# Kernel optimization log

Measured on AMD Instinct MI355X. Metric: run time of the kernel, lower is better.

## Reference

```python
import jax, jax.numpy as jnp
import numpy as np

IMG, P, C, E = 256, 16, 3, 200
N = (IMG // P) ** 2          # 256 patches
NUM_MASKED = int(N * 0.75)   # 192
PATCH_ELEMS = C * P * P      # 768


def setup_inputs() -> dict:
    key = jax.random.key(0)
    ks = jax.random.split(key, 10)
    B = 128
    x = jax.random.normal(ks[0], (B, C, IMG, IMG), dtype=jnp.float32)
    perm = jax.random.permutation(ks[1], N).astype(jnp.int32)
    conv_w = jax.random.normal(ks[2], (E, C, P, P), dtype=jnp.float32) * 0.02
    conv_b = jnp.zeros((E,), dtype=jnp.float32)
    pos_embed = jax.random.normal(ks[3], (1, N, E), dtype=jnp.float32) * 0.02
    mask_token = jnp.zeros((1, E), dtype=jnp.float32)
    W_enc = jax.random.normal(ks[4], (E, E), dtype=jnp.float32) * (1.0 / np.sqrt(E))
    b_enc = jnp.zeros((E,), dtype=jnp.float32)
    W_dec = jax.random.normal(ks[5], (E, PATCH_ELEMS), dtype=jnp.float32) * (1.0 / np.sqrt(E))
    b_dec = jnp.zeros((PATCH_ELEMS,), dtype=jnp.float32)
    return {"x": x, "conv_w": conv_w, "conv_b": conv_b, "pos_embed": pos_embed,
            "mask_token": mask_token, "W_enc": W_enc, "b_enc": b_enc,
            "W_dec": W_dec, "b_dec": b_dec, "perm": perm}


def _patchify(x):
    # [B,C,H,W] -> [B, N, C*P*P], row-major patch order (matches conv stride=P then flatten)
    B = x.shape[0]
    g = IMG // P
    x = x.reshape(B, C, g, P, g, P)           # B C gh P gw P
    x = x.transpose(0, 2, 4, 1, 3, 5)         # B gh gw C P P
    return x.reshape(B, g * g, C * P * P)


def _fold(patches):
    # [B, N, C*P*P] -> [B,C,H,W]; idx iterates rows (i) outer, cols (j) inner
    B = patches.shape[0]
    g = IMG // P
    p = patches.reshape(B, g, g, C, P, P)
    return p.transpose(0, 3, 1, 4, 2, 5).reshape(B, C, IMG, IMG)


def reference(x, conv_w, conv_b, pos_embed, mask_token, W_enc, b_enc, W_dec, b_dec, perm):
    masked_idx = perm[:NUM_MASKED]
    unmasked_idx = perm[NUM_MASKED:]
    # patch embed (Conv2d k=P, stride=P == linear over flattened patches)
    patches = _patchify(x)                                   # [B,N,768]
    w_flat = conv_w.reshape(E, -1)                           # [E, 768]
    emb = jnp.einsum('bnp,ep->bne', patches, w_flat) + conv_b + pos_embed  # [B,N,E]
    visible = emb[:, unmasked_idx, :]                        # [B, N-192, E]
    encoded = jnp.einsum('bne,ef->bnf', visible, W_enc) + b_enc
    B = x.shape[0]
    full = jnp.zeros((B, N, E), dtype=x.dtype)
    full = full.at[:, unmasked_idx, :].set(encoded)
    full = full.at[:, masked_idx, :].set(jnp.broadcast_to(mask_token, (B, NUM_MASKED, E)))
    full = full + pos_embed
    dec = jnp.einsum('bne,ep->bnp', full, W_dec) + b_dec     # [B,N,768]
    img = _fold(dec)                                         # [B,C,H,W]
    return img, masked_idx
```

## Files before the change

### kernel.cpp

```cpp
#include <hip/hip_runtime.h>

typedef __attribute__((ext_vector_type(8))) __bf16 bf16x8;
typedef __attribute__((ext_vector_type(4))) float f32x4;

constexpr int Bsz   = 128;
constexpr int EE    = 200;
constexpr int EP    = 256;
constexpr int KP    = 224;
constexpr int NMASK = 192;
constexpr int PE    = 768;
constexpr int M1    = Bsz * 64;
constexpr long IMG_ELEMS = (long)Bsz * 3 * 256 * 256;

constexpr int VROWS = 16;
constexpr int VBLK  = M1 / VROWS;
constexpr int FBLK  = NMASK * 4;
constexpr int ASTR  = 776;
constexpr int TSTR  = 264;

__device__ __forceinline__ f32x4 mfma16(bf16x8 a, bf16x8 b, f32x4 c) {
    return __builtin_amdgcn_mfma_f32_16x16x32_bf16(a, b, c, 0, 0, 0);
}

__global__ __launch_bounds__(256) void k_prep(
    const float* __restrict__ pos, const float* __restrict__ wflat,
    const float* __restrict__ Wenc, const float* __restrict__ Wdec,
    const float* __restrict__ conv_b, const float* __restrict__ b_enc,
    const float* __restrict__ b_dec, const float* __restrict__ mask_token,
    const int* __restrict__ perm,
    float* __restrict__ posP, __bf16* __restrict__ W1t,
    __bf16* __restrict__ W2t, __bf16* __restrict__ W3t,
    float* __restrict__ cbp, float* __restrict__ bep,
    float* __restrict__ dec_masked, float* __restrict__ out_idx)
{
    __shared__ float rowv[256];
    int blk = blockIdx.x, t = threadIdx.x;
    if (blk < 256) {
        posP[blk * 256 + t] = (t < EE) ? pos[blk * EE + t] : 0.f;
        return;
    }
    blk -= 256;
    if (blk < 768) {
        int e = blk / 3, k = (blk % 3) * 256 + t;
        W1t[e * 768 + k] = (e < EE) ? (__bf16)wflat[e * 768 + k] : (__bf16)0.f;
        return;
    }
    blk -= 768;
    if (blk < 256) {
        if (t < KP) W2t[blk * KP + t] =
            (blk < EE && t < EE) ? (__bf16)Wenc[t * EE + blk] : (__bf16)0.f;
        return;
    }
    blk -= 256;
    if (blk < 768) {
        if (t < KP) W3t[blk * KP + t] =
            (t < EE) ? (__bf16)Wdec[t * PE + blk] : (__bf16)0.f;
        return;
    }
    blk -= 768;
    if (blk < NMASK) {
        const int i = blk;
        const int n = perm[i];
        rowv[t] = (t < EE) ? (mask_token[t] + pos[n * EE + t]) : 0.f;
        __syncthreads();
        float a0 = b_dec[t], a1 = b_dec[t + 256], a2 = b_dec[t + 512];
        #pragma unroll 4
        for (int k = 0; k < EE; ++k) {
            const float rv = rowv[k];
            a0 = fmaf(rv, Wdec[k * PE + t], a0);
            a1 = fmaf(rv, Wdec[k * PE + t + 256], a1);
            a2 = fmaf(rv, Wdec[k * PE + t + 512], a2);
        }
        dec_masked[i * PE + t]       = a0;
        dec_masked[i * PE + t + 256] = a1;
        dec_masked[i * PE + t + 512] = a2;
        return;
    }
    cbp[t] = (t < EE) ? conv_b[t] : 0.f;
    bep[t] = (t < EE) ? b_enc[t] : 0.f;
    if (t < NMASK) out_idx[t] = (float)perm[t];
}

__global__ __launch_bounds__(512, 4) void k_mega(
    const float* __restrict__ x, const __bf16* __restrict__ W1t,
    const __bf16* __restrict__ W2t, const __bf16* __restrict__ W3t,
    const float* __restrict__ cbp, const float* __restrict__ bep,
    const float* __restrict__ posP, const float* __restrict__ bdec,
    const int* __restrict__ perm, const float* __restrict__ dec_masked,
    float* __restrict__ img)
{
    __shared__ __bf16 smem[VROWS * ASTR];
    __bf16* As    = smem;
    __bf16* vis_t = smem;
    __bf16* ful_t = smem + VROWS * TSTR;
    __shared__ int nidx[VROWS];

    const int t    = threadIdx.x;
    const int grp5 = blockIdx.x / 5, rem5 = blockIdx.x % 5;
    const int lane = t & 63, wid = t >> 6;
    const int quad = lane >> 4, lid = lane & 15;

    if (rem5 >= 2) {
        const int fb  = grp5 * 3 + (rem5 - 2);
        const int i   = fb % NMASK;
        const int grp = fb / NMASK;
        const int n   = perm[i];
        if (t < 384) {
            const int sub = t / 192, f4 = t % 192;
            f32x4 v = *(const f32x4*)&dec_masked[i * PE + f4 * 4];
            const int p = f4 * 4;
            const int c = p >> 8, py = (p >> 4) & 15, px = p & 15;
            const long base = (long)c * 65536 + ((n >> 4) * 16 + py) * 256
                            + (n & 15) * 16 + px;
            const int b0 = grp * 32 + sub * 16;
            #pragma unroll
            for (int bb = 0; bb < 16; ++bb)
                __builtin_nontemporal_store(
                    v, (f32x4*)&img[(long)(b0 + bb) * 3 * 65536 + base]);
        }
        return;
    }

    const int bid  = grp5 * 2 + rem5;
    const int m0   = bid * VROWS;
    const int bimg = m0 >> 6;
    if (t < VROWS) nidx[t] = perm[NMASK + (m0 & 63) + t];

    {
        const int row = t >> 5;
        const int tt  = t & 31;
        const int m = m0 + row;
        const int n = perm[NMASK + (m & 63)];
        const int abase = bimg * 196608 + (n >> 4) * 4096 + (n & 15) * 16;
        #pragma unroll
        for (int it = 0; it < 3; ++it) {
            int k = tt * 8 + it * 256;
            int c = k >> 8, py = (k >> 4) & 15, px = k & 15;
            const float* ap = x + abase + c * 65536 + py * 256 + px;
            f32x4 a0 = __builtin_nontemporal_load((const f32x4*)ap);
            f32x4 a1 = __builtin_nontemporal_load((const f32x4*)(ap + 4));
            bf16x8 av;
            av[0] = (__bf16)a0.x; av[1] = (__bf16)a0.y; av[2] = (__bf16)a0.z; av[3] = (__bf16)a0.w;
            av[4] = (__bf16)a1.x; av[5] = (__bf16)a1.y; av[6] = (__bf16)a1.z; av[7] = (__bf16)a1.w;
            *(bf16x8*)&As[row * ASTR + k] = av;
        }
    }
    __syncthreads();

    const int e0w = wid * 32;
    f32x4 acc1[2] = {};
    const __bf16* b1 = &W1t[e0w * 768 + quad * 8];
    #pragma unroll 8
    for (int k0 = 0; k0 < 768; k0 += 32) {
        bf16x8 a0 = *(const bf16x8*)&As[lid * ASTR + k0 + quad * 8];
        #pragma unroll
        for (int j = 0; j < 2; ++j) {
            bf16x8 bv = *(const bf16x8*)&b1[(j * 16 + lid) * 768 + k0];
            acc1[j] = mfma16(a0, bv, acc1[j]);
        }
    }
    __syncthreads();

    #pragma unroll
    for (int j = 0; j < 2; ++j) {
        const int e = e0w + j * 16 + lid;
        const float cb = cbp[e];
        #pragma unroll
        for (int r = 0; r < 4; ++r) {
            const int ml = quad * 4 + r;
            vis_t[ml * TSTR + e] = (__bf16)(acc1[j][r] + cb + posP[nidx[ml] * 256 + e]);
        }
    }
    __syncthreads();

    f32x4 acc2[2] = {};
    const __bf16* b2 = &W2t[e0w * KP + quad * 8];
    #pragma unroll
    for (int k0 = 0; k0 < KP; k0 += 32) {
        bf16x8 a0 = *(const bf16x8*)&vis_t[lid * TSTR + k0 + quad * 8];
        #pragma unroll
        for (int j = 0; j < 2; ++j) {
            bf16x8 bv = *(const bf16x8*)&b2[(j * 16 + lid) * KP + k0];
            acc2[j] = mfma16(a0, bv, acc2[j]);
        }
    }
    #pragma unroll
    for (int j = 0; j < 2; ++j) {
        const int e = e0w + j * 16 + lid;
        const float be = bep[e];
        #pragma unroll
        for (int r = 0; r < 4; ++r) {
            const int ml = quad * 4 + r;
            ful_t[ml * TSTR + e] = (__bf16)(acc2[j][r] + be + posP[nidx[ml] * 256 + e]);
        }
    }
    __syncthreads();

    f32x4 acc3[6] = {};
    const int p0w = wid * 96;
    const __bf16* b3 = &W3t[p0w * KP + quad * 8];
    #pragma unroll
    for (int k0 = 0; k0 < KP; k0 += 32) {
        bf16x8 a0 = *(const bf16x8*)&ful_t[lid * TSTR + k0 + quad * 8];
        #pragma unroll
        for (int j = 0; j < 6; ++j) {
            bf16x8 bv = *(const bf16x8*)&b3[(j * 16 + lid) * KP + k0];
            acc3[j] = mfma16(a0, bv, acc3[j]);
        }
    }
    #pragma unroll
    for (int j = 0; j < 6; ++j) {
        const int p = p0w + j * 16 + lid;
        const int c = p >> 8, py = (p >> 4) & 15, px = p & 15;
        const float bd = bdec[p];
        const long obase = (long)(bimg * 3 + c) * 65536 + py * 256 + px;
        #pragma unroll
        for (int r = 0; r < 4; ++r) {
            const int n = nidx[quad * 4 + r];
            __builtin_nontemporal_store(
                acc3[j][r] + bd, &img[obase + (n >> 4) * 4096 + (n & 15) * 16]);
        }
    }
}

extern "C" void kernel_launch(void* const* d_in, const int* in_sizes, int n_in,
                              void* d_out, int out_size, void* d_ws, size_t ws_size,
                              hipStream_t stream)
{
    const float* x          = (const float*)d_in[0];
    const float* conv_w     = (const float*)d_in[1];
    const float* conv_b     = (const float*)d_in[2];
    const float* pos        = (const float*)d_in[3];
    const float* mask_token = (const float*)d_in[4];
    const float* W_enc      = (const float*)d_in[5];
    const float* b_enc      = (const float*)d_in[6];
    const float* W_dec      = (const float*)d_in[7];
    const float* b_dec      = (const float*)d_in[8];
    const int*   perm       = (const int*)d_in[9];
    float* out = (float*)d_out;

    __bf16* visible = (__bf16*)d_ws;
    __bf16* full    = visible + M1 * EP;
    __bf16* W1t     = full + (M1 + NMASK) * EP;
    __bf16* W2t     = W1t + 256 * 768;
    __bf16* W3t     = W2t + 256 * KP;
    float*  posP    = (float*)(W3t + 768 * KP);
    float*  cbp     = posP + 256 * 256;
    float*  bep     = cbp + 256;
    float*  decm    = bep + 256;

    k_prep<<<256 + 768 + 256 + 768 + NMASK + 1, 256, 0, stream>>>(
        pos, conv_w, W_enc, W_dec, conv_b, b_enc, b_dec, mask_token, perm,
        posP, W1t, W2t, W3t, cbp, bep, decm, out + IMG_ELEMS);
    k_mega<<<VBLK + FBLK, 512, 0, stream>>>(
        x, W1t, W2t, W3t, cbp, bep, posP, b_dec, perm, decm, out);
}
```

Before: 252.3 us.

## Collapse the three linear layers into one precomputed 768x768 weight plus per-patch bias table

```diff
diff --git a/kernel.cpp b/kernel.cpp
--- a/kernel.cpp
+++ b/kernel.cpp
@@ -5,8 +5,6 @@
 
 constexpr int Bsz   = 128;
 constexpr int EE    = 200;
-constexpr int EP    = 256;
-constexpr int KP    = 224;
 constexpr int NMASK = 192;
 constexpr int PE    = 768;
 constexpr int M1    = Bsz * 64;
@@ -16,58 +14,77 @@
 constexpr int VBLK  = M1 / VROWS;
 constexpr int FBLK  = NMASK * 4;
 constexpr int ASTR  = 776;
-constexpr int TSTR  = 264;
 
 __device__ __forceinline__ f32x4 mfma16(bf16x8 a, bf16x8 b, f32x4 c) {
     return __builtin_amdgcn_mfma_f32_16x16x32_bf16(a, b, c, 0, 0, 0);
 }
 
-__global__ __launch_bounds__(256) void k_prep(
-    const float* __restrict__ pos, const float* __restrict__ wflat,
-    const float* __restrict__ Wenc, const float* __restrict__ Wdec,
-    const float* __restrict__ conv_b, const float* __restrict__ b_enc,
-    const float* __restrict__ b_dec, const float* __restrict__ mask_token,
-    const int* __restrict__ perm,
-    float* __restrict__ posP, __bf16* __restrict__ W1t,
-    __bf16* __restrict__ W2t, __bf16* __restrict__ W3t,
-    float* __restrict__ cbp, float* __restrict__ bep,
+__global__ __launch_bounds__(256) void k_prep1(
+    const float* __restrict__ pos, const float* __restrict__ Wenc,
+    const float* __restrict__ Wdec, const float* __restrict__ conv_b,
+    const float* __restrict__ b_enc, const float* __restrict__ b_dec,
+    const float* __restrict__ mask_token, const int* __restrict__ perm,
+    float* __restrict__ W2D, float* __restrict__ T,
     float* __restrict__ dec_masked, float* __restrict__ out_idx)
 {
-    __shared__ float rowv[256];
+    __shared__ float u[256];
+    __shared__ float v[256];
     int blk = blockIdx.x, t = threadIdx.x;
+
+    if (blk < 200) {
+        const int e = blk;
+        if (t < EE) u[t] = Wenc[e * EE + t];
+        __syncthreads();
+        float a0 = 0.f, a1 = 0.f, a2 = 0.f;
+        #pragma unroll 4
+        for (int f = 0; f < EE; ++f) {
+            const float w = u[f];
+            a0 = fmaf(w, Wdec[f * PE + t],       a0);
+            a1 = fmaf(w, Wdec[f * PE + t + 256], a1);
+            a2 = fmaf(w, Wdec[f * PE + t + 512], a2);
+        }
+        W2D[e * PE + t]       = a0;
+        W2D[e * PE + t + 256] = a1;
+        W2D[e * PE + t + 512] = a2;
+        return;
+    }
+    blk -= 200;
     if (blk < 256) {
-        posP[blk * 256 + t] = (t < EE) ? pos[blk * EE + t] : 0.f;
+        const int n = blk;
+        if (t < EE) u[t] = conv_b[t] + pos[n * EE + t];
+        __syncthreads();
+        if (t < EE) {
+            float a = 0.f;
+            #pragma unroll 4
+            for (int e = 0; e < EE; ++e)
+                a = fmaf(u[e], Wenc[e * EE + t], a);
+            v[t] = a + b_enc[t] + pos[n * EE + t];
+        }
+        __syncthreads();
+        float a0 = b_dec[t], a1 = b_dec[t + 256], a2 = b_dec[t + 512];
+        #pragma unroll 4
+        for (int f = 0; f < EE; ++f) {
+            const float w = v[f];
+            a0 = fmaf(w, Wdec[f * PE + t],       a0);
+            a1 = fmaf(w, Wdec[f * PE + t + 256], a1);
+            a2 = fmaf(w, Wdec[f * PE + t + 512], a2);
+        }
+        T[n * PE + t]       = a0;
+        T[n * PE + t + 256] = a1;
+        T[n * PE + t + 512] = a2;
         return;
     }
     blk -= 256;
-    if (blk < 768) {
-        int e = blk / 3, k = (blk % 3) * 256 + t;
-        W1t[e * 768 + k] = (e < EE) ? (__bf16)wflat[e * 768 + k] : (__bf16)0.f;
-        return;
-    }
-    blk -= 768;
-    if (blk < 256) {
-        if (t < KP) W2t[blk * KP + t] =
-            (blk < EE && t < EE) ? (__bf16)Wenc[t * EE + blk] : (__bf16)0.f;
-        return;
-    }
-    blk -= 256;
-    if (blk < 768) {
-        if (t < KP) W3t[blk * KP + t] =
-            (t < EE) ? (__bf16)Wdec[t * PE + blk] : (__bf16)0.f;
-        return;
-    }
-    blk -= 768;
     if (blk < NMASK) {
         const int i = blk;
         const int n = perm[i];
-        rowv[t] = (t < EE) ? (mask_token[t] + pos[n * EE + t]) : 0.f;
+        u[t] = (t < EE) ? (mask_token[t] + pos[n * EE + t]) : 0.f;
         __syncthreads();
         float a0 = b_dec[t], a1 = b_dec[t + 256], a2 = b_dec[t + 512];
         #pragma unroll 4
         for (int k = 0; k < EE; ++k) {
-            const float rv = rowv[k];
-            a0 = fmaf(rv, Wdec[k * PE + t], a0);
+            const float rv = u[k];
+            a0 = fmaf(rv, Wdec[k * PE + t],       a0);
             a1 = fmaf(rv, Wdec[k * PE + t + 256], a1);
             a2 = fmaf(rv, Wdec[k * PE + t + 512], a2);
         }
@@ -76,32 +93,44 @@
         dec_masked[i * PE + t + 512] = a2;
         return;
     }
-    cbp[t] = (t < EE) ? conv_b[t] : 0.f;
-    bep[t] = (t < EE) ? b_enc[t] : 0.f;
     if (t < NMASK) out_idx[t] = (float)perm[t];
 }
 
+__global__ __launch_bounds__(256) void k_prep2(
+    const float* __restrict__ wflat, const float* __restrict__ W2D,
+    __bf16* __restrict__ W123t)
+{
+    __shared__ float colv[256];
+    const int p = blockIdx.x, t = threadIdx.x;
+    if (t < EE) colv[t] = W2D[t * PE + p];
+    __syncthreads();
+    float a0 = 0.f, a1 = 0.f, a2 = 0.f;
+    #pragma unroll 4
+    for (int e = 0; e < EE; ++e) {
+        const float w = colv[e];
+        a0 = fmaf(w, wflat[e * PE + t],       a0);
+        a1 = fmaf(w, wflat[e * PE + t + 256], a1);
+        a2 = fmaf(w, wflat[e * PE + t + 512], a2);
+    }
+    W123t[p * PE + t]       = (__bf16)a0;
+    W123t[p * PE + t + 256] = (__bf16)a1;
+    W123t[p * PE + t + 512] = (__bf16)a2;
+}
+
 __global__ __launch_bounds__(512, 4) void k_mega(
-    const float* __restrict__ x, const __bf16* __restrict__ W1t,
-    const __bf16* __restrict__ W2t, const __bf16* __restrict__ W3t,
-    const float* __restrict__ cbp, const float* __restrict__ bep,
-    const float* __restrict__ posP, const float* __restrict__ bdec,
-    const int* __restrict__ perm, const float* __restrict__ dec_masked,
-    float* __restrict__ img)
-{
-    __shared__ __bf16 smem[VROWS * ASTR];
-    __bf16* As    = smem;
-    __bf16* vis_t = smem;
-    __bf16* ful_t = smem + VROWS * TSTR;
+    const float* __restrict__ x, const __bf16* __restrict__ W123t,
+    const float* __restrict__ T, const int* __restrict__ perm,
+    const float* __restrict__ dec_masked, float* __restrict__ img)
+{
+    __shared__ __bf16 As[VROWS * ASTR];
     __shared__ int nidx[VROWS];
 
     const int t    = threadIdx.x;
-    const int grp5 = blockIdx.x / 5, rem5 = blockIdx.x % 5;
     const int lane = t & 63, wid = t >> 6;
     const int quad = lane >> 4, lid = lane & 15;
 
-    if (rem5 >= 2) {
-        const int fb  = grp5 * 3 + (rem5 - 2);
+    if (blockIdx.x < FBLK) {
+        const int fb  = blockIdx.x;
         const int i   = fb % NMASK;
         const int grp = fb / NMASK;
         const int n   = perm[i];
@@ -121,7 +150,7 @@
         return;
     }
 
-    const int bid  = grp5 * 2 + rem5;
+    const int bid  = blockIdx.x - FBLK;
     const int m0   = bid * VROWS;
     const int bimg = m0 >> 6;
     if (t < VROWS) nidx[t] = perm[NMASK + (m0 & 63) + t];
@@ -147,78 +176,42 @@
     }
     __syncthreads();
 
-    const int e0w = wid * 32;
-    f32x4 acc1[2] = {};
-    const __bf16* b1 = &W1t[e0w * 768 + quad * 8];
-    #pragma unroll 8
-    for (int k0 = 0; k0 < 768; k0 += 32) {
+    const int p0w = wid * 96;
+    f32x4 acc[6] = {};
+    const __bf16* bp0 = &W123t[(p0w + 0 * 16 + lid) * PE + quad * 8];
+    const __bf16* bp1 = &W123t[(p0w + 1 * 16 + lid) * PE + quad * 8];
+    const __bf16* bp2 = &W123t[(p0w + 2 * 16 + lid) * PE + quad * 8];
+    const __bf16* bp3 = &W123t[(p0w + 3 * 16 + lid) * PE + quad * 8];
+    const __bf16* bp4 = &W123t[(p0w + 4 * 16 + lid) * PE + quad * 8];
+    const __bf16* bp5 = &W123t[(p0w + 5 * 16 + lid) * PE + quad * 8];
+    #pragma unroll 2
+    for (int k0 = 0; k0 < PE; k0 += 32) {
         bf16x8 a0 = *(const bf16x8*)&As[lid * ASTR + k0 + quad * 8];
-        #pragma unroll
-        for (int j = 0; j < 2; ++j) {
-            bf16x8 bv = *(const bf16x8*)&b1[(j * 16 + lid) * 768 + k0];
-            acc1[j] = mfma16(a0, bv, acc1[j]);
-        }
-    }
-    __syncthreads();
-
-    #pragma unroll
-    for (int j = 0; j < 2; ++j) {
-        const int e = e0w + j * 16 + lid;
-        const float cb = cbp[e];
-        #pragma unroll
-        for (int r = 0; r < 4; ++r) {
-            const int ml = quad * 4 + r;
-            vis_t[ml * TSTR + e] = (__bf16)(acc1[j][r] + cb + posP[nidx[ml] * 256 + e]);
-        }
-    }
-    __syncthreads();
-
-    f32x4 acc2[2] = {};
-    const __bf16* b2 = &W2t[e0w * KP + quad * 8];
-    #pragma unroll
-    for (int k0 = 0; k0 < KP; k0 += 32) {
-        bf16x8 a0 = *(const bf16x8*)&vis_t[lid * TSTR + k0 + quad * 8];
-        #pragma unroll
-        for (int j = 0; j < 2; ++j) {
-            bf16x8 bv = *(const bf16x8*)&b2[(j * 16 + lid) * KP + k0];
-            acc2[j] = mfma16(a0, bv, acc2[j]);
-        }
-    }
-    #pragma unroll
-    for (int j = 0; j < 2; ++j) {
-        const int e = e0w + j * 16 + lid;
-        const float be = bep[e];
-        #pragma unroll
-        for (int r = 0; r < 4; ++r) {
-            const int ml = quad * 4 + r;
-            ful_t[ml * TSTR + e] = (__bf16)(acc2[j][r] + be + posP[nidx[ml] * 256 + e]);
-        }
-    }
-    __syncthreads();
-
-    f32x4 acc3[6] = {};
-    const int p0w = wid * 96;
-    const __bf16* b3 = &W3t[p0w * KP + quad * 8];
-    #pragma unroll
-    for (int k0 = 0; k0 < KP; k0 += 32) {
-        bf16x8 a0 = *(const bf16x8*)&ful_t[lid * TSTR + k0 + quad * 8];
-        #pragma unroll
-        for (int j = 0; j < 6; ++j) {
-            bf16x8 bv = *(const bf16x8*)&b3[(j * 16 + lid) * KP + k0];
-            acc3[j] = mfma16(a0, bv, acc3[j]);
-        }
-    }
+        bf16x8 b0 = *(const bf16x8*)&bp0[k0];
+        bf16x8 b1 = *(const bf16x8*)&bp1[k0];
+        bf16x8 b2 = *(const bf16x8*)&bp2[k0];
+        bf16x8 b3 = *(const bf16x8*)&bp3[k0];
+        bf16x8 b4 = *(const bf16x8*)&bp4[k0];
+        bf16x8 b5 = *(const bf16x8*)&bp5[k0];
+        acc[0] = mfma16(a0, b0, acc[0]);
+        acc[1] = mfma16(a0, b1, acc[1]);
+        acc[2] = mfma16(a0, b2, acc[2]);
+        acc[3] = mfma16(a0, b3, acc[3]);
+        acc[4] = mfma16(a0, b4, acc[4]);
+        acc[5] = mfma16(a0, b5, acc[5]);
+    }
+
     #pragma unroll
     for (int j = 0; j < 6; ++j) {
         const int p = p0w + j * 16 + lid;
         const int c = p >> 8, py = (p >> 4) & 15, px = p & 15;
-        const float bd = bdec[p];
         const long obase = (long)(bimg * 3 + c) * 65536 + py * 256 + px;
         #pragma unroll
         for (int r = 0; r < 4; ++r) {
             const int n = nidx[quad * 4 + r];
+            const float v = acc[j][r] + T[n * PE + p];
             __builtin_nontemporal_store(
-                acc3[j][r] + bd, &img[obase + (n >> 4) * 4096 + (n & 15) * 16]);
+                v, &img[obase + (n >> 4) * 4096 + (n & 15) * 16]);
         }
     }
 }
@@ -239,19 +232,15 @@
     const int*   perm       = (const int*)d_in[9];
     float* out = (float*)d_out;
 
-    __bf16* visible = (__bf16*)d_ws;
-    __bf16* full    = visible + M1 * EP;
-    __bf16* W1t     = full + (M1 + NMASK) * EP;
-    __bf16* W2t     = W1t + 256 * 768;
-    __bf16* W3t     = W2t + 256 * KP;
-    float*  posP    = (float*)(W3t + 768 * KP);
-    float*  cbp     = posP + 256 * 256;
-    float*  bep     = cbp + 256;
-    float*  decm    = bep + 256;
-
-    k_prep<<<256 + 768 + 256 + 768 + NMASK + 1, 256, 0, stream>>>(
-        pos, conv_w, W_enc, W_dec, conv_b, b_enc, b_dec, mask_token, perm,
-        posP, W1t, W2t, W3t, cbp, bep, decm, out + IMG_ELEMS);
-    k_mega<<<VBLK + FBLK, 512, 0, stream>>>(
-        x, W1t, W2t, W3t, cbp, bep, posP, b_dec, perm, decm, out);
-}
+    __bf16* W123t = (__bf16*)d_ws;
+    float*  W2D   = (float*)(W123t + PE * PE);
+    float*  T     = W2D + EE * PE;
+    float*  decm  = T + 256 * PE;
+
+    k_prep1<<<200 + 256 + NMASK + 1, 256, 0, stream>>>(
+        pos, W_enc, W_dec, conv_b, b_enc, b_dec, mask_token, perm,
+        W2D, T, decm, out + IMG_ELEMS);
+    k_prep2<<<PE, 256, 0, stream>>>(conv_w, W2D, W123t);
+    k_mega<<<FBLK + VBLK, 512, 0, stream>>>(
+        x, W123t, T, perm, decm, out);
+}
```

Result: slower. 306.2 us (+21.4%).
